# Optimization experiments

Measured on AMD Instinct MI355X. Metric: run time of the kernel, lower is better.

## Reference

```python
import jax, jax.numpy as jnp
import numpy as np

B, L, D_MODEL, D_INNER, D_CONV = 4, 4096, 1024, 2048, 4


def setup_inputs() -> dict:
    key = jax.random.key(0)
    ks = jax.random.split(key, 9)
    r = lambda k, shape, s: jax.random.normal(k, shape, dtype=jnp.float32) * s
    return {
        "x": r(ks[0], (B, L, D_MODEL), 1.0),
        "Wi": r(ks[1], (2 * D_INNER, D_MODEL), 0.02),        # in_proj (no bias)
        "Wconv": r(ks[2], (D_INNER, 1, D_CONV), 0.2),        # depthwise conv1d weight
        "bconv": r(ks[3], (D_INNER,), 0.02),                 # conv1d bias
        "Wdt": r(ks[4], (D_INNER, D_INNER), 0.01),           # dt_proj weight
        "bdt": jnp.full((D_INNER,), -3.0, jnp.float32),     # dt_proj bias -> small dt
        "WB": r(ks[5], (D_INNER, D_INNER), 0.02),            # B_proj
        "WC": r(ks[6], (D_INNER, D_INNER), 0.02),            # C_proj
        "Wo": r(ks[7], (D_MODEL, D_INNER), 0.02),            # out_proj
        "A_log": jnp.log(jnp.full((D_INNER,), 0.1, jnp.float32)),
    }


def reference(x, Wi, Wconv, bconv, Wdt, bdt, WB, WC, Wo, A_log):
    L_ = x.shape[1]
    d_conv = Wconv.shape[-1]
    d_inner = Wconv.shape[0]

    # in_proj and gate split
    xz = jnp.einsum('bld,ed->ble', x, Wi)          # [B, L, 2*d_inner]
    x1, z = jnp.split(xz, 2, axis=-1)

    # depthwise causal conv1d (padding=d_conv-1 then truncate == left-pad only)
    xc = jax.lax.conv_general_dilated(
        jnp.transpose(x1, (0, 2, 1)), Wconv,
        window_strides=(1,), padding=[(d_conv - 1, 0)],
        dimension_numbers=('NCH', 'OIH', 'NCH'),
        feature_group_count=d_inner) + bconv[None, :, None]
    xc = jnp.transpose(jax.nn.silu(xc), (0, 2, 1))  # [B, L, d_inner]

    dt = jax.nn.softplus(jnp.einsum('ble,fe->blf', xc, Wdt) + bdt)
    B_t = jax.nn.sigmoid(jnp.einsum('ble,fe->blf', xc, WB))
    C_t = jnp.tanh(jnp.einsum('ble,fe->blf', xc, WC))
    u_t = xc * B_t

    A = -jnp.exp(A_log)                              # [d_inner], negative
    log_alpha = jnp.clip(A[None, None, :] * dt, -10.0, -0.0001)
    S = jnp.cumsum(log_alpha, axis=1)                # [B, L, d_inner]

    u_prev = jnp.concatenate([jnp.zeros_like(u_t[:, :1]), u_t[:, :-1]], axis=1)
    beta = dt * 0.5 * (u_prev + u_t)                 # trapezoid input term

    # stabilized log-cumsum-exp style parallel scan
    m = jnp.max(-S, axis=1, keepdims=True)
    h = jnp.exp(S + m) * jnp.cumsum(beta * jnp.exp(-S - m), axis=1)

    y = h * C_t * jax.nn.silu(z)
    return jnp.einsum('blf,df->bld', y, Wo)
```

## Files before the change

kernel.cpp:

```cpp
#include <hip/hip_runtime.h>
#include <cstdint>

typedef unsigned short u16;
typedef unsigned int u32;
typedef __bf16 bf16x8 __attribute__((ext_vector_type(8)));
typedef float f32x4 __attribute__((ext_vector_type(4)));
typedef unsigned short u16x8 __attribute__((ext_vector_type(8)));

#define BM 128
#define BN 128
#define BK 32
#define CL 32
#define NC 128
#define VCH 8
#define DI 2048
#define DM 1024
#define LSEQ 4096

__device__ __forceinline__ float bf2f(u16 u) {
    union { uint32_t i; float f; } v; v.i = ((uint32_t)u) << 16; return v.f;
}
__device__ __forceinline__ u16 f2bf(float f) {
    union { float f; uint32_t i; } v; v.f = f;
    uint32_t r = v.i + 0x7fffu + ((v.i >> 16) & 1u);
    return (u16)(r >> 16);
}

__device__ __forceinline__ void gl_lds16(const u16* g, u16* l) {
    __builtin_amdgcn_global_load_lds(
        (const __attribute__((address_space(1))) u32*)g,
        (__attribute__((address_space(3))) u32*)l, 16, 0, 0);
}

__global__ __launch_bounds__(256)
void cast_f2b(const float* __restrict__ src, u16* __restrict__ dst, long n)
{
    long i = ((long)blockIdx.x * 256 + threadIdx.x) * 8;
    if (i >= n) return;
    float4 v0 = *(const float4*)(src + i);
    float4 v1 = *(const float4*)(src + i + 4);
    u16x8 o;
    o[0] = f2bf(v0.x); o[1] = f2bf(v0.y); o[2] = f2bf(v0.z); o[3] = f2bf(v0.w);
    o[4] = f2bf(v1.x); o[5] = f2bf(v1.y); o[6] = f2bf(v1.z); o[7] = f2bf(v1.w);
    *(u16x8*)(dst + i) = o;
}

template<int EPI>
__global__ __launch_bounds__(256, 4)
void gemm_bt(const u16* __restrict__ A, const u16* __restrict__ W,
             int M, int N, int K,
             const float* __restrict__ auxf,
             const u16* __restrict__ auxb,
             u16* __restrict__ ob0, u16* __restrict__ ob1,
             u16* __restrict__ ob2, float* __restrict__ outf)
{
    __shared__ __align__(16) u16 As[BM * BK];
    __shared__ __align__(16) u16 Bs[BN * BK];

    const int t    = threadIdx.x;
    const int lane = t & 63;
    const int w    = t >> 6;
    const int quad = lane >> 4;
    const int l16  = lane & 15;
    const int wm   = w >> 1, wn = w & 1;
    const long m0  = (long)blockIdx.y * BM;
    const long n0  = (long)blockIdx.x * BN;

    const int rr = lane >> 2;
    const int cg = ((lane & 3) - ((lane >> 3) & 3)) & 3;

    const u16* gA0 = A + (size_t)(m0 + (2 * w)     * 16 + rr) * K + cg * 8;
    const u16* gA1 = A + (size_t)(m0 + (2 * w + 1) * 16 + rr) * K + cg * 8;
    const u16* gB0 = W + (size_t)(n0 + (2 * w)     * 16 + rr) * K + cg * 8;
    const u16* gB1 = W + (size_t)(n0 + (2 * w + 1) * 16 + rr) * K + cg * 8;

    u16* lA0 = As + (2 * w)     * 512;
    u16* lA1 = As + (2 * w + 1) * 512;
    u16* lB0 = Bs + (2 * w)     * 512;
    u16* lB1 = Bs + (2 * w + 1) * 512;

    const int slotr = (quad + (l16 >> 1)) & 3;
    const u16* rdA = As + (wm * 64 + l16) * 32 + slotr * 8;
    const u16* rdB = Bs + (wn * 64 + l16) * 32 + slotr * 8;

    f32x4 acc[4][4];
#pragma unroll
    for (int i = 0; i < 4; ++i)
#pragma unroll
        for (int j = 0; j < 4; ++j)
            acc[i][j] = (f32x4){0.f, 0.f, 0.f, 0.f};

    for (int k0 = 0; k0 < K; k0 += BK) {
        __syncthreads();
        gl_lds16(gA0 + k0, lA0);
        gl_lds16(gA1 + k0, lA1);
        gl_lds16(gB0 + k0, lB0);
        gl_lds16(gB1 + k0, lB1);
        __syncthreads();

        bf16x8 af[4], bfr[4];
#pragma unroll
        for (int fi = 0; fi < 4; ++fi)
            af[fi] = *(const bf16x8*)(rdA + fi * 512);
#pragma unroll
        for (int fj = 0; fj < 4; ++fj)
            bfr[fj] = *(const bf16x8*)(rdB + fj * 512);
#pragma unroll
        for (int i = 0; i < 4; ++i)
#pragma unroll
            for (int j = 0; j < 4; ++j)
                acc[i][j] = __builtin_amdgcn_mfma_f32_16x16x32_bf16(af[i], bfr[j], acc[i][j], 0, 0, 0);
    }

#pragma unroll
    for (int i = 0; i < 4; ++i) {
#pragma unroll
        for (int j = 0; j < 4; ++j) {
            const long nc = n0 + wn * 64 + j * 16 + l16;
#pragma unroll
            for (int rg = 0; rg < 4; ++rg) {
                const long mr = m0 + wm * 64 + i * 16 + quad * 4 + rg;
                float v = acc[i][j][rg];
                if (EPI == 0) {
                    if (nc < DI) ob0[mr * DI + nc] = f2bf(v);
                    else         ob1[mr * DI + (nc - DI)] = f2bf(v);
                } else if (EPI == 1) {
                    const int  g   = (int)(nc >> 11);
                    const long col = nc & (DI - 1);
                    if (g == 0) {
                        v += auxf[col];
                        float sp = (v > 20.f) ? v : log1pf(expf(v));
                        ob0[mr * DI + col] = f2bf(sp);
                    } else if (g == 1) {
                        float bt  = 1.f / (1.f + expf(-v));
                        float xcv = bf2f(auxb[mr * DI + col]);
                        ob1[mr * DI + col] = f2bf(xcv * bt);
                    } else {
                        ob2[mr * DI + col] = f2bf(tanhf(v));
                    }
                } else {
                    outf[mr * DM + nc] = v;
                }
            }
        }
    }
}

__global__ __launch_bounds__(256)
void conv_silu(const u16* __restrict__ x1, const float* __restrict__ Wc,
               const float* __restrict__ bc, u16* __restrict__ xc)
{
    const long bl = blockIdx.x;
    const int  l  = (int)(bl & (LSEQ - 1));
    const int  d0 = threadIdx.x * VCH;
    const size_t base = (size_t)bl * DI + d0;

    float acc[VCH];
    {
        float4 b0 = *(const float4*)(bc + d0);
        float4 b1 = *(const float4*)(bc + d0 + 4);
        acc[0] = b0.x; acc[1] = b0.y; acc[2] = b0.z; acc[3] = b0.w;
        acc[4] = b1.x; acc[5] = b1.y; acc[6] = b1.z; acc[7] = b1.w;
    }
    float wv[VCH][4];
#pragma unroll
    for (int v = 0; v < VCH; ++v) {
        float4 t = *(const float4*)(Wc + (size_t)(d0 + v) * 4);
        wv[v][0] = t.x; wv[v][1] = t.y; wv[v][2] = t.z; wv[v][3] = t.w;
    }

#pragma unroll
    for (int tp = 0; tp < 4; ++tp) {
        const int ls = l - 3 + tp;
        if (ls >= 0) {
            u16x8 vx = *(const u16x8*)(x1 + base + (long)(tp - 3) * DI);
#pragma unroll
            for (int v = 0; v < VCH; ++v)
                acc[v] += bf2f(vx[v]) * wv[v][tp];
        }
    }
    u16x8 o;
#pragma unroll
    for (int v = 0; v < VCH; ++v) {
        float s = acc[v] / (1.f + expf(-acc[v]));
        o[v] = f2bf(s);
    }
    *(u16x8*)(xc + base) = o;
}

__global__ __launch_bounds__(256)
void scan_a(const u16* __restrict__ dt, const u16* __restrict__ u,
            const float* __restrict__ A_log,
            float* __restrict__ sumlog, float* __restrict__ hend, int nbD)
{
    const int d0 = threadIdx.x * VCH;
    const int b  = blockIdx.y;
    const int c  = blockIdx.z;
    float Ad[VCH];
    {
        float4 a0 = *(const float4*)(A_log + d0);
        float4 a1 = *(const float4*)(A_log + d0 + 4);
        Ad[0] = -expf(a0.x); Ad[1] = -expf(a0.y); Ad[2] = -expf(a0.z); Ad[3] = -expf(a0.w);
        Ad[4] = -expf(a1.x); Ad[5] = -expf(a1.y); Ad[6] = -expf(a1.z); Ad[7] = -expf(a1.w);
    }
    size_t base = ((size_t)b * LSEQ + (size_t)c * CL) * DI + d0;

    float pu[VCH], sl[VCH], h[VCH];
    if (c == 0) {
#pragma unroll
        for (int v = 0; v < VCH; ++v) pu[v] = 0.f;
    } else {
        u16x8 vp = *(const u16x8*)(u + base - DI);
#pragma unroll
        for (int v = 0; v < VCH; ++v) pu[v] = bf2f(vp[v]);
    }
#pragma unroll
    for (int v = 0; v < VCH; ++v) { sl[v] = 0.f; h[v] = 0.f; }

    u16x8 vdt = *(const u16x8*)(dt + base);
    u16x8 vu  = *(const u16x8*)(u  + base);
    for (int s = 0; s < CL; ++s) {
        u16x8 ndt = *(const u16x8*)(dt + base + DI);
        u16x8 nu  = *(const u16x8*)(u  + base + DI);
#pragma unroll
        for (int v = 0; v < VCH; ++v) {
            float dtv = bf2f(vdt[v]);
            float uv  = bf2f(vu[v]);
            float la  = fminf(fmaxf(Ad[v] * dtv, -10.f), -1e-4f);
            sl[v] += la;
            h[v] = expf(la) * h[v] + dtv * 0.5f * (pu[v] + uv);
            pu[v] = uv;
        }
        vdt = ndt; vu = nu;
        base += DI;
    }
    const size_t chn = (size_t)c * nbD + b * DI + d0;
    *(float4*)(sumlog + chn)     = (float4){sl[0], sl[1], sl[2], sl[3]};
    *(float4*)(sumlog + chn + 4) = (float4){sl[4], sl[5], sl[6], sl[7]};
    *(float4*)(hend   + chn)     = (float4){h[0], h[1], h[2], h[3]};
    *(float4*)(hend   + chn + 4) = (float4){h[4], h[5], h[6], h[7]};
}

__global__ __launch_bounds__(256)
void scan_b(const float* __restrict__ sumlog, const float* __restrict__ hend,
            float* __restrict__ hin, int nbD)
{
    const int chn = blockIdx.x * 256 + threadIdx.x;
    float carry = 0.f;
#pragma unroll 4
    for (int c = 0; c < NC; ++c) {
        hin[(size_t)c * nbD + chn] = carry;
        carry = expf(sumlog[(size_t)c * nbD + chn]) * carry + hend[(size_t)c * nbD + chn];
    }
}

__global__ __launch_bounds__(256)
void scan_c(const u16* __restrict__ dt, const u16* __restrict__ u,
            const float* __restrict__ A_log, const float* __restrict__ hin,
            const u16* __restrict__ Ct, const u16* __restrict__ z,
            u16* __restrict__ y, int nbD)
{
    const int d0 = threadIdx.x * VCH;
    const int b  = blockIdx.y;
    const int c  = blockIdx.z;
    float Ad[VCH];
    {
        float4 a0 = *(const float4*)(A_log + d0);
        float4 a1 = *(const float4*)(A_log + d0 + 4);
        Ad[0] = -expf(a0.x); Ad[1] = -expf(a0.y); Ad[2] = -expf(a0.z); Ad[3] = -expf(a0.w);
        Ad[4] = -expf(a1.x); Ad[5] = -expf(a1.y); Ad[6] = -expf(a1.z); Ad[7] = -expf(a1.w);
    }
    size_t base = ((size_t)b * LSEQ + (size_t)c * CL) * DI + d0;
    const size_t chn = (size_t)c * nbD + b * DI + d0;

    float h[VCH], pu[VCH];
    {
        float4 h0 = *(const float4*)(hin + chn);
        float4 h1 = *(const float4*)(hin + chn + 4);
        h[0] = h0.x; h[1] = h0.y; h[2] = h0.z; h[3] = h0.w;
        h[4] = h1.x; h[5] = h1.y; h[6] = h1.z; h[7] = h1.w;
    }
    if (c == 0) {
#pragma unroll
        for (int v = 0; v < VCH; ++v) pu[v] = 0.f;
    } else {
        u16x8 vp = *(const u16x8*)(u + base - DI);
#pragma unroll
        for (int v = 0; v < VCH; ++v) pu[v] = bf2f(vp[v]);
    }

    u16x8 vdt = *(const u16x8*)(dt + base);
    u16x8 vu  = *(const u16x8*)(u  + base);
    u16x8 vct = *(const u16x8*)(Ct + base);
    u16x8 vz  = *(const u16x8*)(z  + base);
    for (int s = 0; s < CL; ++s) {
        u16x8 ndt = *(const u16x8*)(dt + base + DI);
        u16x8 nu  = *(const u16x8*)(u  + base + DI);
        u16x8 nct = *(const u16x8*)(Ct + base + DI);
        u16x8 nz  = *(const u16x8*)(z  + base + DI);
        u16x8 o;
#pragma unroll
        for (int v = 0; v < VCH; ++v) {
            float dtv = bf2f(vdt[v]);
            float uv  = bf2f(vu[v]);
            float la  = fminf(fmaxf(Ad[v] * dtv, -10.f), -1e-4f);
            h[v] = expf(la) * h[v] + dtv * 0.5f * (pu[v] + uv);
            pu[v] = uv;
            float ct = bf2f(vct[v]);
            float zv = bf2f(vz[v]);
            float sz = zv / (1.f + expf(-zv));
            o[v] = f2bf(h[v] * ct * sz);
        }
        *(u16x8*)(y + base) = o;
        vdt = ndt; vu = nu; vct = nct; vz = nz;
        base += DI;
    }
}

struct WeightsB {
    const u16 *Wi, *Wcat, *Wo;
};
struct SmallF {
    const float *Wconv, *bconv, *bdt, *A_log;
};

static void run_pipeline(int nb, const float* x, float* out, char* ws,
                         const WeightsB& wb, const SmallF& sf, hipStream_t stream)
{
    const int Mrows = nb * LSEQ;
    const size_t nE = (size_t)Mrows * DI;
    const size_t nX = (size_t)Mrows * DM;
    const int nbD = nb * DI;

    char* p = ws;
    u16* b0 = (u16*)p; p += nE * 2;
    u16* b1 = (u16*)p; p += nE * 2;
    u16* b2 = (u16*)p; p += nE * 2;
    u16* b3 = (u16*)p; p += nE * 2;
    u16* b4 = (u16*)p; p += nE * 2;

    u16* xb = b2;
    u16* x1 = b0; u16* z = b1; u16* xc = b2;
    u16* dt = b0; u16* u  = b3; u16* Ct = b4; u16* y = b4;

    float* sumlog = (float*)b2;
    float* hend   = sumlog + (size_t)nbD * NC;
    float* hin    = hend   + (size_t)nbD * NC;

    dim3 blk(256);

    cast_f2b<<<dim3((unsigned)(nX / 2048)), blk, 0, stream>>>(x, xb, (long)nX);

    gemm_bt<0><<<dim3(2 * DI / BN, Mrows / BM), blk, 0, stream>>>(
        xb, wb.Wi, Mrows, 2 * DI, DM, nullptr, nullptr, x1, z, nullptr, nullptr);

    conv_silu<<<dim3((unsigned)Mrows), blk, 0, stream>>>(x1, sf.Wconv, sf.bconv, xc);

    gemm_bt<1><<<dim3(3 * DI / BN, Mrows / BM), blk, 0, stream>>>(
        xc, wb.Wcat, Mrows, 3 * DI, DI, sf.bdt, xc, dt, u, Ct, nullptr);

    scan_a<<<dim3(1, nb, NC), blk, 0, stream>>>(dt, u, sf.A_log, sumlog, hend, nbD);
    scan_b<<<dim3(nbD / 256), blk, 0, stream>>>(sumlog, hend, hin, nbD);
    scan_c<<<dim3(1, nb, NC), blk, 0, stream>>>(dt, u, sf.A_log, hin, Ct, z, y, nbD);

    gemm_bt<2><<<dim3(DM / BN, Mrows / BM), blk, 0, stream>>>(
        y, wb.Wo, Mrows, DM, DI, nullptr, nullptr, nullptr, nullptr, nullptr, out);
}

extern "C" void kernel_launch(void* const* d_in, const int* in_sizes, int n_in,
                              void* d_out, int out_size, void* d_ws, size_t ws_size,
                              hipStream_t stream)
{
    const float* x     = (const float*)d_in[0];
    const float* Wi    = (const float*)d_in[1];
    const float* Wconv = (const float*)d_in[2];
    const float* bconv = (const float*)d_in[3];
    const float* Wdt   = (const float*)d_in[4];
    const float* bdt   = (const float*)d_in[5];
    const float* WB    = (const float*)d_in[6];
    const float* WC    = (const float*)d_in[7];
    const float* Wo    = (const float*)d_in[8];
    const float* A_log = (const float*)d_in[9];

    const size_t nWi = (size_t)2 * DI * DM;
    const size_t nWp = (size_t)DI * DI;
    const size_t nWo = (size_t)DM * DI;

    const size_t wbytes = (nWi + 3 * nWp + nWo) * 2;
    char* q = (char*)d_ws + ws_size - wbytes;
    u16* Wi_b   = (u16*)q; q += nWi * 2;
    u16* Wcat_b = (u16*)q; q += 3 * nWp * 2;
    u16* Wo_b   = (u16*)q; q += nWo * 2;

    dim3 blk(256);
    cast_f2b<<<dim3((unsigned)(nWi / 2048)), blk, 0, stream>>>(Wi,  Wi_b, (long)nWi);
    cast_f2b<<<dim3((unsigned)(nWp / 2048)), blk, 0, stream>>>(Wdt, Wcat_b,            (long)nWp);
    cast_f2b<<<dim3((unsigned)(nWp / 2048)), blk, 0, stream>>>(WB,  Wcat_b + nWp,      (long)nWp);
    cast_f2b<<<dim3((unsigned)(nWp / 2048)), blk, 0, stream>>>(WC,  Wcat_b + 2 * nWp,  (long)nWp);
    cast_f2b<<<dim3((unsigned)(nWo / 2048)), blk, 0, stream>>>(Wo,  Wo_b, (long)nWo);

    WeightsB wb{Wi_b, Wcat_b, Wo_b};
    SmallF   sf{Wconv, bconv, bdt, A_log};

    auto need = [&](int nb) -> size_t {
        size_t nE = (size_t)nb * LSEQ * DI;
        return 5 * nE * 2;
    };

    if (ws_size >= need(4) + wbytes) {
        run_pipeline(4, x, (float*)d_out, (char*)d_ws, wb, sf, stream);
    } else if (ws_size >= need(2) + wbytes) {
        for (int b = 0; b < 4; b += 2)
            run_pipeline(2, x + (size_t)b * LSEQ * DM,
                         (float*)d_out + (size_t)b * LSEQ * DM,
                         (char*)d_ws, wb, sf, stream);
    } else {
        for (int b = 0; b < 4; ++b)
            run_pipeline(1, x + (size_t)b * LSEQ * DM,
                         (float*)d_out + (size_t)b * LSEQ * DM,
                         (char*)d_ws, wb, sf, stream);
    }
}
```

Measured before the change: 1.371 ms.

## Process two K-slabs per GEMM barrier pair, specialize kernels, fuse weight casts

The GEMM main loop now loads two BK=32 slabs into doubled LDS buffers before each barrier pair and runs both slabs of MFMAs. This halves the number of __syncthreads per K and gives the load unit more work in flight per barrier, at the cost of twice the LDS per block, which may limit occupancy. The templated GEMM is split into three named kernels with fewer parameters. The five weight-cast launches are merged into one kernel, cutting launch overhead.

```diff
diff --git a/kernel.cpp b/kernel.cpp
--- a/kernel.cpp
+++ b/kernel.cpp
@@ -10,6 +10,7 @@
 #define BM 128
 #define BN 128
 #define BK 32
+#define PL (BM * BK)
 #define CL 32
 #define NC 128
 #define VCH 8
@@ -45,17 +46,39 @@
     *(u16x8*)(dst + i) = o;
 }
 
+__global__ __launch_bounds__(256)
+void cast_weights(const float* __restrict__ Wi, const float* __restrict__ Wdt,
+                  const float* __restrict__ WB, const float* __restrict__ WC,
+                  const float* __restrict__ Wo,
+                  u16* __restrict__ Wi_b, u16* __restrict__ Wcat_b,
+                  u16* __restrict__ Wo_b)
+{
+    const long nWi = (long)2 * DI * DM;
+    const long nWp = (long)DI * DI;
+    long i = ((long)blockIdx.x * 256 + threadIdx.x) * 8;
+    const float* src; u16* dst; long off;
+    if (i < nWi)                  { src = Wi;  dst = Wi_b;            off = i; }
+    else if (i < nWi + nWp)       { src = Wdt; dst = Wcat_b;          off = i - nWi; }
+    else if (i < nWi + 2 * nWp)   { src = WB;  dst = Wcat_b + nWp;    off = i - nWi - nWp; }
+    else if (i < nWi + 3 * nWp)   { src = WC;  dst = Wcat_b + 2*nWp;  off = i - nWi - 2*nWp; }
+    else                          { src = Wo;  dst = Wo_b;            off = i - nWi - 3*nWp; }
+    float4 v0 = *(const float4*)(src + off);
+    float4 v1 = *(const float4*)(src + off + 4);
+    u16x8 o;
+    o[0] = f2bf(v0.x); o[1] = f2bf(v0.y); o[2] = f2bf(v0.z); o[3] = f2bf(v0.w);
+    o[4] = f2bf(v1.x); o[5] = f2bf(v1.y); o[6] = f2bf(v1.z); o[7] = f2bf(v1.w);
+    *(u16x8*)(dst + off) = o;
+}
+
 template<int EPI>
-__global__ __launch_bounds__(256, 4)
-void gemm_bt(const u16* __restrict__ A, const u16* __restrict__ W,
-             int M, int N, int K,
-             const float* __restrict__ auxf,
-             const u16* __restrict__ auxb,
+__device__ __forceinline__ void gemm_body(
+             const u16* __restrict__ A, const u16* __restrict__ W, int K,
+             const float* __restrict__ auxf, const u16* __restrict__ auxb,
              u16* __restrict__ ob0, u16* __restrict__ ob1,
              u16* __restrict__ ob2, float* __restrict__ outf)
 {
-    __shared__ __align__(16) u16 As[BM * BK];
-    __shared__ __align__(16) u16 Bs[BN * BK];
+    __shared__ __align__(16) u16 As[2 * BM * BK];
+    __shared__ __align__(16) u16 Bs[2 * BN * BK];
 
     const int t    = threadIdx.x;
     const int lane = t & 63;
@@ -90,26 +113,35 @@
         for (int j = 0; j < 4; ++j)
             acc[i][j] = (f32x4){0.f, 0.f, 0.f, 0.f};
 
-    for (int k0 = 0; k0 < K; k0 += BK) {
+    for (int k0 = 0; k0 < K; k0 += 2 * BK) {
         __syncthreads();
         gl_lds16(gA0 + k0, lA0);
         gl_lds16(gA1 + k0, lA1);
+        gl_lds16(gA0 + k0 + BK, lA0 + PL);
+        gl_lds16(gA1 + k0 + BK, lA1 + PL);
         gl_lds16(gB0 + k0, lB0);
         gl_lds16(gB1 + k0, lB1);
+        gl_lds16(gB0 + k0 + BK, lB0 + PL);
+        gl_lds16(gB1 + k0 + BK, lB1 + PL);
         __syncthreads();
 
-        bf16x8 af[4], bfr[4];
-#pragma unroll
-        for (int fi = 0; fi < 4; ++fi)
-            af[fi] = *(const bf16x8*)(rdA + fi * 512);
-#pragma unroll
-        for (int fj = 0; fj < 4; ++fj)
-            bfr[fj] = *(const bf16x8*)(rdB + fj * 512);
-#pragma unroll
-        for (int i = 0; i < 4; ++i)
-#pragma unroll
-            for (int j = 0; j < 4; ++j)
-                acc[i][j] = __builtin_amdgcn_mfma_f32_16x16x32_bf16(af[i], bfr[j], acc[i][j], 0, 0, 0);
+#pragma unroll
+        for (int kk = 0; kk < 2; ++kk) {
+            const u16* pA = rdA + kk * PL;
+            const u16* pB = rdB + kk * PL;
+            bf16x8 af[4], bfr[4];
+#pragma unroll
+            for (int fi = 0; fi < 4; ++fi)
+                af[fi] = *(const bf16x8*)(pA + fi * 512);
+#pragma unroll
+            for (int fj = 0; fj < 4; ++fj)
+                bfr[fj] = *(const bf16x8*)(pB + fj * 512);
+#pragma unroll
+            for (int i = 0; i < 4; ++i)
+#pragma unroll
+                for (int j = 0; j < 4; ++j)
+                    acc[i][j] = __builtin_amdgcn_mfma_f32_16x16x32_bf16(af[i], bfr[j], acc[i][j], 0, 0, 0);
+        }
     }
 
 #pragma unroll
@@ -146,6 +178,26 @@
     }
 }
 
+__global__ __launch_bounds__(256, 4)
+void gemm_in(const u16* __restrict__ A, const u16* __restrict__ W, int K,
+             u16* __restrict__ ob0, u16* __restrict__ ob1)
+{
+    gemm_body<0>(A, W, K, nullptr, nullptr, ob0, ob1, nullptr, nullptr);
+}
+__global__ __launch_bounds__(256, 4)
+void gemm_dbc(const u16* __restrict__ A, const u16* __restrict__ W, int K,
+              const float* __restrict__ auxf, const u16* __restrict__ auxb,
+              u16* __restrict__ ob0, u16* __restrict__ ob1, u16* __restrict__ ob2)
+{
+    gemm_body<1>(A, W, K, auxf, auxb, ob0, ob1, ob2, nullptr);
+}
+__global__ __launch_bounds__(256, 4)
+void gemm_out(const u16* __restrict__ A, const u16* __restrict__ W, int K,
+              float* __restrict__ outf)
+{
+    gemm_body<2>(A, W, K, nullptr, nullptr, nullptr, nullptr, nullptr, outf);
+}
+
 __global__ __launch_bounds__(256)
 void conv_silu(const u16* __restrict__ x1, const float* __restrict__ Wc,
                const float* __restrict__ bc, u16* __restrict__ xc)
@@ -351,20 +403,20 @@
 
     cast_f2b<<<dim3((unsigned)(nX / 2048)), blk, 0, stream>>>(x, xb, (long)nX);
 
-    gemm_bt<0><<<dim3(2 * DI / BN, Mrows / BM), blk, 0, stream>>>(
-        xb, wb.Wi, Mrows, 2 * DI, DM, nullptr, nullptr, x1, z, nullptr, nullptr);
+    gemm_in<<<dim3(2 * DI / BN, Mrows / BM), blk, 0, stream>>>(
+        xb, wb.Wi, DM, x1, z);
 
     conv_silu<<<dim3((unsigned)Mrows), blk, 0, stream>>>(x1, sf.Wconv, sf.bconv, xc);
 
-    gemm_bt<1><<<dim3(3 * DI / BN, Mrows / BM), blk, 0, stream>>>(
-        xc, wb.Wcat, Mrows, 3 * DI, DI, sf.bdt, xc, dt, u, Ct, nullptr);
+    gemm_dbc<<<dim3(3 * DI / BN, Mrows / BM), blk, 0, stream>>>(
+        xc, wb.Wcat, DI, sf.bdt, xc, dt, u, Ct);
 
     scan_a<<<dim3(1, nb, NC), blk, 0, stream>>>(dt, u, sf.A_log, sumlog, hend, nbD);
     scan_b<<<dim3(nbD / 256), blk, 0, stream>>>(sumlog, hend, hin, nbD);
     scan_c<<<dim3(1, nb, NC), blk, 0, stream>>>(dt, u, sf.A_log, hin, Ct, z, y, nbD);
 
-    gemm_bt<2><<<dim3(DM / BN, Mrows / BM), blk, 0, stream>>>(
-        y, wb.Wo, Mrows, DM, DI, nullptr, nullptr, nullptr, nullptr, nullptr, out);
+    gemm_out<<<dim3(DM / BN, Mrows / BM), blk, 0, stream>>>(
+        y, wb.Wo, DI, out);
 }
 
 extern "C" void kernel_launch(void* const* d_in, const int* in_sizes, int n_in,
@@ -393,11 +445,11 @@
     u16* Wo_b   = (u16*)q; q += nWo * 2;
 
     dim3 blk(256);
-    cast_f2b<<<dim3((unsigned)(nWi / 2048)), blk, 0, stream>>>(Wi,  Wi_b, (long)nWi);
-    cast_f2b<<<dim3((unsigned)(nWp / 2048)), blk, 0, stream>>>(Wdt, Wcat_b,            (long)nWp);
-    cast_f2b<<<dim3((unsigned)(nWp / 2048)), blk, 0, stream>>>(WB,  Wcat_b + nWp,      (long)nWp);
-    cast_f2b<<<dim3((unsigned)(nWp / 2048)), blk, 0, stream>>>(WC,  Wcat_b + 2 * nWp,  (long)nWp);
-    cast_f2b<<<dim3((unsigned)(nWo / 2048)), blk, 0, stream>>>(Wo,  Wo_b, (long)nWo);
+    {
+        const long nW = (long)(nWi + 3 * nWp + nWo);
+        cast_weights<<<dim3((unsigned)(nW / 2048)), blk, 0, stream>>>(
+            Wi, Wdt, WB, WC, Wo, Wi_b, Wcat_b, Wo_b);
+    }
 
     WeightsB wb{Wi_b, Wcat_b, Wo_b};
     SmallF   sf{Wconv, bconv, bdt, A_log};
```

Result: faster. 1.271 ms (-7.3%).
